# Performance work log

Hardware: AMD Instinct MI355X
Metric: run time of the kernel (lower is better)

## Reference

```python
import jax, jax.numpy as jnp
import numpy as np

B, S, D_IN, H = 64, 1024, 1024, 1024


def setup_inputs() -> dict:
    key = jax.random.key(0)
    ks = jax.random.split(key, 5)
    scale_x = 1.0 / np.sqrt(D_IN)
    scale_h = 1.0 / np.sqrt(H)
    # gate order along leading axis: f, i, o, g
    W = jax.random.uniform(ks[0], (4, D_IN, H), jnp.float32, -scale_x, scale_x)
    bW = jax.random.uniform(ks[1], (4, H), jnp.float32, -scale_x, scale_x)
    U = jax.random.uniform(ks[2], (4, H, H), jnp.float32, -scale_h, scale_h)
    bU = jax.random.uniform(ks[3], (4, H), jnp.float32, -scale_h, scale_h)
    input_emb = jax.random.normal(ks[4], (B, S, D_IN), jnp.float32)
    return {"input_emb": input_emb, "W": W, "bW": bW, "U": U, "bU": bU}


def reference(input_emb, W, bW, U, bU):
    b, s, _ = input_emb.shape
    h_dim = W.shape[-1]
    # Precompute input projections for all 4 gates across all timesteps: (S, B, 4, H)
    xproj = jnp.einsum('bsd,kdh->sbkh', input_emb, W) + bW

    def step(carry, xt):
        h_prev, c_prev = carry
        # recurrent projection for all gates: (B, 4, H)
        gates = xt + jnp.einsum('bh,kho->bko', h_prev, U) + bU
        f_t = jax.nn.sigmoid(gates[:, 0])
        i_t = jax.nn.sigmoid(gates[:, 1])
        o_t = jax.nn.sigmoid(gates[:, 2])
        g_t = jax.nn.sigmoid(gates[:, 3])  # NOTE: original uses sigmoid here, not tanh
        c_t = f_t * c_prev + i_t * g_t
        h_t = o_t * jnp.tanh(c_t)
        return (h_t, c_t), h_t

    h0 = jnp.zeros((b, h_dim), input_emb.dtype)
    c0 = jnp.zeros((b, h_dim), input_emb.dtype)
    (h_last, c_last), ys = jax.lax.scan(step, (h0, c0), xproj)
    outputs = jnp.transpose(ys, (1, 0, 2))  # (B, S, H)
    return outputs, (h_last, c_last)
```

## Files before the change

### kernel.cpp

```cpp
#include <hip/hip_runtime.h>
#include <hip/hip_bf16.h>
#include <stdint.h>


typedef __attribute__((ext_vector_type(8))) short short8;
typedef __attribute__((ext_vector_type(4))) float floatx4;
typedef __attribute__((ext_vector_type(2))) float floatx2;

__device__ __forceinline__ unsigned short f2bf(float x){
  union { float f; unsigned int u; } v; v.f = x;
  unsigned int r = v.u + 0x7fffu + ((v.u >> 16) & 1u);
  return (unsigned short)(r >> 16);
}
__device__ __forceinline__ float bf2f(unsigned short b){
  union { unsigned int u; float f; } v; v.u = ((unsigned int)b) << 16; return v.f;
}
__device__ __forceinline__ float fsigmoid(float x){ return 1.0f / (1.0f + __expf(-x)); }
__device__ __forceinline__ float ftanh(float x){ return 1.0f - 2.0f / (1.0f + __expf(2.0f * x)); }

__global__ void k_transpose_bf16(const float* __restrict__ src, unsigned short* __restrict__ dst){
  __shared__ float tile[64][65];
  const int g  = blockIdx.z;
  const int d0 = blockIdx.x * 64;
  const int h0 = blockIdx.y * 64;
  const int t  = threadIdx.x;
  const float* s    = src + ((size_t)g << 20);
  unsigned short* o = dst + ((size_t)g << 20);
  #pragma unroll
  for (int i = 0; i < 16; i++){
    int e = i * 256 + t;
    int r = e >> 6, c = e & 63;
    tile[r][c] = s[(size_t)(d0 + r) * 1024 + (h0 + c)];
  }
  __syncthreads();
  #pragma unroll
  for (int i = 0; i < 16; i++){
    int e = i * 256 + t;
    int a = e >> 6, bb = e & 63;
    o[(size_t)(h0 + a) * 1024 + (d0 + bb)] = f2bf(tile[bb][a]);
  }
}

__global__ void k_convert_x(const float* __restrict__ inp, unsigned short* __restrict__ abuf, int s0){
  int idx = blockIdx.x * 256 + threadIdx.x;
  int e = idx * 4;
  int r = e >> 10, d = e & 1023;
  int b = r & 63, sl = r >> 6;
  floatx4 v = *(const floatx4*)(inp + ((size_t)(b * 1024 + (s0 + sl)) * 1024 + d));
  unsigned long long pk = (unsigned long long)f2bf(v[0])
                        | ((unsigned long long)f2bf(v[1]) << 16)
                        | ((unsigned long long)f2bf(v[2]) << 32)
                        | ((unsigned long long)f2bf(v[3]) << 48);
  *(unsigned long long*)(abuf + (size_t)r * 1024 + d) = pk;
}

__global__ void __launch_bounds__(256) k_gemm_xproj(
    const unsigned short* __restrict__ A,
    const unsigned short* __restrict__ Bt,
    const float* __restrict__ bW,
    const float* __restrict__ bU,
    unsigned short* __restrict__ Cc)
{
  __shared__ unsigned short As[2][128][64];
  __shared__ unsigned short Bs[2][128][64];
  const int t = threadIdx.x;
  const int w = t >> 6;
  const int lane = t & 63;
  const int m0 = blockIdx.x * 128;
  const int n0 = blockIdx.y * 128;
  floatx4 acc[4][4];
  #pragma unroll
  for (int i = 0; i < 4; i++)
    #pragma unroll
    for (int j = 0; j < 4; j++)
      acc[i][j] = (floatx4){0.f, 0.f, 0.f, 0.f};

  auto stage = [&](int bufi, int kt){
    #pragma unroll
    for (int i = 0; i < 4; i++){
      int chunk = i * 256 + t;
      int r = chunk >> 3, j = chunk & 7;
      int js = j ^ (r & 7);
      __builtin_amdgcn_global_load_lds(
        (const __attribute__((address_space(1))) unsigned int*)(A + (size_t)(m0 + r) * 1024 + kt * 64 + js * 8),
        (__attribute__((address_space(3))) unsigned int*)(&As[bufi][0][0] + (i * 256 + w * 64) * 8), 16, 0, 0);
    }
    #pragma unroll
    for (int i = 0; i < 4; i++){
      int chunk = i * 256 + t;
      int r = chunk >> 3, j = chunk & 7;
      int js = j ^ (r & 7);
      __builtin_amdgcn_global_load_lds(
        (const __attribute__((address_space(1))) unsigned int*)(Bt + (size_t)(n0 + r) * 1024 + kt * 64 + js * 8),
        (__attribute__((address_space(3))) unsigned int*)(&Bs[bufi][0][0] + (i * 256 + w * 64) * 8), 16, 0, 0);
    }
  };

  auto compute = [&](int bufi){
    const int mi0 = (w >> 1) * 64;
    const int ni0 = (w & 1) * 64;
    #pragma unroll
    for (int kc = 0; kc < 2; kc++){
      short8 af[4], bfr[4];
      #pragma unroll
      for (int mi = 0; mi < 4; mi++){
        int row = mi0 + mi * 16 + (lane & 15);
        int j = kc * 4 + (lane >> 4);
        af[mi] = *(const short8*)&As[bufi][row][(j ^ (row & 7)) * 8];
      }
      #pragma unroll
      for (int ni = 0; ni < 4; ni++){
        int row = ni0 + ni * 16 + (lane & 15);
        int j = kc * 4 + (lane >> 4);
        bfr[ni] = *(const short8*)&Bs[bufi][row][(j ^ (row & 7)) * 8];
      }
      #pragma unroll
      for (int mi = 0; mi < 4; mi++)
        #pragma unroll
        for (int ni = 0; ni < 4; ni++)
          acc[mi][ni] = __builtin_amdgcn_mfma_f32_16x16x32_bf16(af[mi], bfr[ni], acc[mi][ni], 0, 0, 0);
    }
  };

  stage(0, 0);
  int buf = 0;
  for (int kt = 0; kt < 16; kt++){
    __syncthreads();
    if (kt < 15) stage(buf ^ 1, kt + 1);
    compute(buf);
    buf ^= 1;
  }

  {
    const int mi0 = (w >> 1) * 64;
    const int ni0 = (w & 1) * 64;
    #pragma unroll
    for (int ni = 0; ni < 4; ni++){
      int col = n0 + ni0 + ni * 16 + (lane & 15);
      float bias = bW[col] + bU[col];
      #pragma unroll
      for (int mi = 0; mi < 4; mi++){
        int mrow = m0 + mi0 + mi * 16 + (lane >> 4) * 4;
        #pragma unroll
        for (int r = 0; r < 4; r++)
          Cc[(size_t)(mrow + r) * 4096 + col] = f2bf(acc[mi][ni][r] + bias);
      }
    }
  }
}

__global__ void __launch_bounds__(256, 1) k_lstm_rec(
    const unsigned short* __restrict__ xp,
    const unsigned short* __restrict__ Ut,
    unsigned short* hbs,
    float* cstate,
    float* __restrict__ out,
    float* __restrict__ hlast,
    float* __restrict__ clast,
    int* flags,
    int s_base, int SC)
{
  const int t = threadIdx.x;
  const int w = t >> 6;
  const int lane = t & 63;
  const int wgid = blockIdx.x;
  const int g  = wgid & 3;
  const int j  = wgid >> 2;
  const int B0 = g * 16;
  const int gc0 = j * 32;

  __shared__ float glds[4][16][33];

  short8 bfrag0[32], bfrag1[32];
  {
    const unsigned short* bp0 = Ut + (size_t)(w * 1024 + gc0 + (lane & 15)) * 1024 + (lane >> 4) * 8;
    const unsigned short* bp1 = bp0 + (size_t)16 * 1024;
    #pragma unroll
    for (int kc = 0; kc < 32; kc++){
      bfrag0[kc] = *(const short8*)(bp0 + kc * 32);
      bfrag1[kc] = *(const short8*)(bp1 + kc * 32);
    }
  }

  const int b   = t >> 4;
  const int cc2 = (t & 15) * 2;
  floatx2 cst;
  if (s_base == 0) cst = (floatx2){0.f, 0.f};
  else             cst = *(const floatx2*)&cstate[(size_t)(B0 + b) * 1024 + gc0 + cc2];

  int bail = 20000000;
  const int fb = g * 32;

  for (int sl = 0; sl < SC; sl++){
    const int s = s_base + sl;
    const int p = s & 1;

    unsigned int xu[4];
    {
      const unsigned short* xr = xp + ((size_t)(sl * 64 + B0 + b)) * 4096 + gc0 + cc2;
      #pragma unroll
      for (int gg = 0; gg < 4; gg++) xu[gg] = *(const unsigned int*)(xr + gg * 1024);
    }
    __builtin_amdgcn_sched_barrier(0);

    const char* gsrc = (const char*)hbs + ((size_t)p * 4 + g) * 32768;
    floatx4 acc0 = (floatx4){0.f,0.f,0.f,0.f};
    floatx4 acc1 = (floatx4){0.f,0.f,0.f,0.f};

    auto wait_chunk = [&](int c){
      if (s == 0) return;
      const int* fp2 = &flags[fb + c * 8 + (lane & 7)];
      while (true){
        int v = __hip_atomic_load(fp2, __ATOMIC_RELAXED, __HIP_MEMORY_SCOPE_AGENT);
        if (__all(v >= s)) break;
        __builtin_amdgcn_s_sleep(1);
        if (--bail < 0) break;
      }
    };

    unsigned long long loA[8], hiA[8], loB[8], hiB[8];
    auto issue8 = [&](unsigned long long (&lo)[8], unsigned long long (&hi)[8], int ch){
      #pragma unroll
      for (int i = 0; i < 8; i++){
        const unsigned long long* sp2 = (const unsigned long long*)(gsrc + (ch * 8 + i) * 1024 + lane * 16);
        lo[i] = __hip_atomic_load(sp2,     __ATOMIC_RELAXED, __HIP_MEMORY_SCOPE_AGENT);
        hi[i] = __hip_atomic_load(sp2 + 1, __ATOMIC_RELAXED, __HIP_MEMORY_SCOPE_AGENT);
      }
    };
    auto crunch8 = [&](unsigned long long (&lo)[8], unsigned long long (&hi)[8], int ch){
      #pragma unroll
      for (int i = 0; i < 8; i++){
        union { unsigned long long q[2]; short8 v; } u;
        u.q[0] = lo[i]; u.q[1] = hi[i];
        acc0 = __builtin_amdgcn_mfma_f32_16x16x32_bf16(u.v, bfrag0[ch * 8 + i], acc0, 0, 0, 0);
        acc1 = __builtin_amdgcn_mfma_f32_16x16x32_bf16(u.v, bfrag1[ch * 8 + i], acc1, 0, 0, 0);
      }
    };
    wait_chunk(0);
    issue8(loA, hiA, 0);
    wait_chunk(1);
    issue8(loB, hiB, 1);
    crunch8(loA, hiA, 0);
    wait_chunk(2);
    issue8(loA, hiA, 2);
    crunch8(loB, hiB, 1);
    wait_chunk(3);
    issue8(loB, hiB, 3);
    crunch8(loA, hiA, 2);
    crunch8(loB, hiB, 3);

    {
      const int r0 = (lane >> 4) * 4;
      const int cl = lane & 15;
      #pragma unroll
      for (int r = 0; r < 4; r++){
        glds[w][r0 + r][cl]      = acc0[r];
        glds[w][r0 + r][16 + cl] = acc1[r];
      }
    }
    __syncthreads();

    float hout[2];
    #pragma unroll
    for (int d = 0; d < 2; d++){
      float fv = fsigmoid(glds[0][b][cc2 + d] + bf2f((unsigned short)(xu[0] >> (16 * d))));
      float iv = fsigmoid(glds[1][b][cc2 + d] + bf2f((unsigned short)(xu[1] >> (16 * d))));
      float ov = fsigmoid(glds[2][b][cc2 + d] + bf2f((unsigned short)(xu[2] >> (16 * d))));
      float gv = fsigmoid(glds[3][b][cc2 + d] + bf2f((unsigned short)(xu[3] >> (16 * d))));
      float cv = fv * cst[d] + iv * gv;
      cst[d] = cv;
      hout[d] = ov * ftanh(cv);
    }

    {
      unsigned int hv = (unsigned int)f2bf(hout[0]) | ((unsigned int)f2bf(hout[1]) << 16);
      unsigned int* dst = (unsigned int*)((char*)hbs + ((size_t)(p ^ 1) * 4 + g) * 32768 + j * 1024
                + (((cc2 >> 3) * 16 + b) << 4) + ((cc2 & 7) << 1));
      __hip_atomic_store(dst, hv, __ATOMIC_RELAXED, __HIP_MEMORY_SCOPE_AGENT);
    }

    if (s == 1023){
      *(floatx2*)&hlast[(size_t)(B0 + b) * 1024 + gc0 + cc2] = (floatx2){hout[0], hout[1]};
      *(floatx2*)&clast[(size_t)(B0 + b) * 1024 + gc0 + cc2] = cst;
    }

    asm volatile("s_waitcnt vmcnt(0)" ::: "memory");
    __syncthreads();
    if (t == 0)
      __hip_atomic_store(&flags[fb + j], s + 1, __ATOMIC_RELAXED, __HIP_MEMORY_SCOPE_AGENT);

    *(floatx2*)&out[((size_t)(B0 + b) * 1024 + s) * 1024 + gc0 + cc2] = (floatx2){hout[0], hout[1]};
  }

  *(floatx2*)&cstate[(size_t)(B0 + b) * 1024 + gc0 + cc2] = cst;
}

extern "C" void kernel_launch(void* const* d_in, const int* in_sizes, int n_in,
                              void* d_out, int out_size, void* d_ws, size_t ws_size,
                              hipStream_t stream)
{
  (void)in_sizes; (void)n_in; (void)out_size;
  const float* input_emb = (const float*)d_in[0];
  const float* W   = (const float*)d_in[1];
  const float* bWp = (const float*)d_in[2];
  const float* U   = (const float*)d_in[3];
  const float* bUp = (const float*)d_in[4];
  float* out   = (float*)d_out;
  float* hlast = out + (size_t)64 * 1024 * 1024;
  float* clast = hlast + 64 * 1024;

  char* base = (char*)d_ws;
  unsigned short* Wt  = (unsigned short*)base;  base += 8388608;
  unsigned short* Ut  = (unsigned short*)base;  base += 8388608;
  unsigned short* hbs = (unsigned short*)base;  base += 262144;
  float* cstate       = (float*)base;           base += 262144;
  int* flags          = (int*)base;             base += 8192;
  size_t fixed = (size_t)(base - (char*)d_ws);
  size_t avail = ws_size > fixed ? ws_size - fixed : 0;
  int SC = 1024;
  while (SC > 8 && (size_t)SC * 655360ull > avail) SC >>= 1;
  unsigned short* Abuf = (unsigned short*)base; base += (size_t)SC * 131072;
  unsigned short* xpb  = (unsigned short*)base;

  hipMemsetAsync(flags, 0, 8192, stream);
  hipMemsetAsync(hbs, 0, 262144, stream);

  k_transpose_bf16<<<dim3(16, 16, 4), 256, 0, stream>>>(W, Wt);
  k_transpose_bf16<<<dim3(16, 16, 4), 256, 0, stream>>>(U, Ut);

  int nch = 1024 / SC;
  for (int cc = 0; cc < nch; cc++){
    int s0 = cc * SC;
    k_convert_x<<<SC * 64, 256, 0, stream>>>(input_emb, Abuf, s0);
    k_gemm_xproj<<<dim3(SC / 2, 32), 256, 0, stream>>>(Abuf, Wt, bWp, bUp, xpb);
    k_lstm_rec<<<128, 256, 0, stream>>>(xpb, Ut, hbs, cstate, out, hlast, clast, flags, s0, SC);
  }
}
```

Baseline: 6.319 ms.

## Split recurrent LSTM across 256 workgroups with 16 hidden columns each

The persistent recurrent kernel now gives each workgroup 16 hidden columns instead of 32 and launches 256 workgroups instead of 128. This halves the register-resident U fragments and the MFMA work per workgroup per timestep, spreading the serial recurrence over more compute units. In exchange, each step waits on twice as many producer flags (16 per chunk instead of 8), and paired h values are packed with a lane shuffle before the store. It relies on all 256 workgroups being co-resident for the spin-wait synchronisation.

```diff
diff --git a/kernel.cpp b/kernel.cpp
--- a/kernel.cpp
+++ b/kernel.cpp
@@ -5,7 +5,6 @@
 
 typedef __attribute__((ext_vector_type(8))) short short8;
 typedef __attribute__((ext_vector_type(4))) float floatx4;
-typedef __attribute__((ext_vector_type(2))) float floatx2;
 
 __device__ __forceinline__ unsigned short f2bf(float x){
   union { float f; unsigned int u; } v; v.f = x;
@@ -167,55 +166,55 @@
   const int g  = wgid & 3;
   const int j  = wgid >> 2;
   const int B0 = g * 16;
-  const int gc0 = j * 32;
-
-  __shared__ float glds[4][16][33];
-
-  short8 bfrag0[32], bfrag1[32];
+  const int gc0 = j * 16;
+
+  __shared__ float glds[4][16][17];
+
+  short8 bfrag[32];
   {
-    const unsigned short* bp0 = Ut + (size_t)(w * 1024 + gc0 + (lane & 15)) * 1024 + (lane >> 4) * 8;
-    const unsigned short* bp1 = bp0 + (size_t)16 * 1024;
-    #pragma unroll
-    for (int kc = 0; kc < 32; kc++){
-      bfrag0[kc] = *(const short8*)(bp0 + kc * 32);
-      bfrag1[kc] = *(const short8*)(bp1 + kc * 32);
-    }
-  }
-
-  const int b   = t >> 4;
-  const int cc2 = (t & 15) * 2;
-  floatx2 cst;
-  if (s_base == 0) cst = (floatx2){0.f, 0.f};
-  else             cst = *(const floatx2*)&cstate[(size_t)(B0 + b) * 1024 + gc0 + cc2];
+    const unsigned short* bp = Ut + (size_t)(w * 1024 + gc0 + (lane & 15)) * 1024 + (lane >> 4) * 8;
+    #pragma unroll
+    for (int kc = 0; kc < 32; kc++)
+      bfrag[kc] = *(const short8*)(bp + kc * 32);
+  }
+
+  const int b  = t >> 4;
+  const int cc = t & 15;
+  float cst;
+  if (s_base == 0) cst = 0.f;
+  else             cst = cstate[(size_t)(B0 + b) * 1024 + gc0 + cc];
 
   int bail = 20000000;
-  const int fb = g * 32;
+  const int fb = g * 64;
 
   for (int sl = 0; sl < SC; sl++){
     const int s = s_base + sl;
     const int p = s & 1;
 
-    unsigned int xu[4];
+    unsigned short xv[4];
     {
-      const unsigned short* xr = xp + ((size_t)(sl * 64 + B0 + b)) * 4096 + gc0 + cc2;
-      #pragma unroll
-      for (int gg = 0; gg < 4; gg++) xu[gg] = *(const unsigned int*)(xr + gg * 1024);
+      const unsigned short* xr = xp + ((size_t)(sl * 64 + B0 + b)) * 4096 + gc0 + cc;
+      #pragma unroll
+      for (int gg = 0; gg < 4; gg++) xv[gg] = xr[gg * 1024];
     }
     __builtin_amdgcn_sched_barrier(0);
 
     const char* gsrc = (const char*)hbs + ((size_t)p * 4 + g) * 32768;
-    floatx4 acc0 = (floatx4){0.f,0.f,0.f,0.f};
-    floatx4 acc1 = (floatx4){0.f,0.f,0.f,0.f};
+    floatx4 acc = (floatx4){0.f,0.f,0.f,0.f};
 
     auto wait_chunk = [&](int c){
       if (s == 0) return;
-      const int* fp2 = &flags[fb + c * 8 + (lane & 7)];
       while (true){
-        int v = __hip_atomic_load(fp2, __ATOMIC_RELAXED, __HIP_MEMORY_SCOPE_AGENT);
-        if (__all(v >= s)) break;
+        bool ok = true;
+        if (lane < 16){
+          int v = __hip_atomic_load(&flags[fb + c * 16 + lane], __ATOMIC_RELAXED, __HIP_MEMORY_SCOPE_AGENT);
+          ok = (v >= s);
+        }
+        if (__all(ok)) break;
         __builtin_amdgcn_s_sleep(1);
         if (--bail < 0) break;
       }
+      asm volatile("" ::: "memory");
     };
 
     unsigned long long loA[8], hiA[8], loB[8], hiB[8];
@@ -232,10 +231,10 @@
       for (int i = 0; i < 8; i++){
         union { unsigned long long q[2]; short8 v; } u;
         u.q[0] = lo[i]; u.q[1] = hi[i];
-        acc0 = __builtin_amdgcn_mfma_f32_16x16x32_bf16(u.v, bfrag0[ch * 8 + i], acc0, 0, 0, 0);
-        acc1 = __builtin_amdgcn_mfma_f32_16x16x32_bf16(u.v, bfrag1[ch * 8 + i], acc1, 0, 0, 0);
+        acc = __builtin_amdgcn_mfma_f32_16x16x32_bf16(u.v, bfrag[ch * 8 + i], acc, 0, 0, 0);
       }
     };
+
     wait_chunk(0);
     issue8(loA, hiA, 0);
     wait_chunk(1);
@@ -253,35 +252,32 @@
       const int r0 = (lane >> 4) * 4;
       const int cl = lane & 15;
       #pragma unroll
-      for (int r = 0; r < 4; r++){
-        glds[w][r0 + r][cl]      = acc0[r];
-        glds[w][r0 + r][16 + cl] = acc1[r];
-      }
+      for (int r = 0; r < 4; r++)
+        glds[w][r0 + r][cl] = acc[r];
     }
     __syncthreads();
 
-    float hout[2];
-    #pragma unroll
-    for (int d = 0; d < 2; d++){
-      float fv = fsigmoid(glds[0][b][cc2 + d] + bf2f((unsigned short)(xu[0] >> (16 * d))));
-      float iv = fsigmoid(glds[1][b][cc2 + d] + bf2f((unsigned short)(xu[1] >> (16 * d))));
-      float ov = fsigmoid(glds[2][b][cc2 + d] + bf2f((unsigned short)(xu[2] >> (16 * d))));
-      float gv = fsigmoid(glds[3][b][cc2 + d] + bf2f((unsigned short)(xu[3] >> (16 * d))));
-      float cv = fv * cst[d] + iv * gv;
-      cst[d] = cv;
-      hout[d] = ov * ftanh(cv);
-    }
+    float fv = fsigmoid(glds[0][b][cc] + bf2f(xv[0]));
+    float iv = fsigmoid(glds[1][b][cc] + bf2f(xv[1]));
+    float ov = fsigmoid(glds[2][b][cc] + bf2f(xv[2]));
+    float gv = fsigmoid(glds[3][b][cc] + bf2f(xv[3]));
+    cst = fv * cst + iv * gv;
+    float hout = ov * ftanh(cst);
 
     {
-      unsigned int hv = (unsigned int)f2bf(hout[0]) | ((unsigned int)f2bf(hout[1]) << 16);
-      unsigned int* dst = (unsigned int*)((char*)hbs + ((size_t)(p ^ 1) * 4 + g) * 32768 + j * 1024
-                + (((cc2 >> 3) * 16 + b) << 4) + ((cc2 & 7) << 1));
-      __hip_atomic_store(dst, hv, __ATOMIC_RELAXED, __HIP_MEMORY_SCOPE_AGENT);
+      unsigned int my = (unsigned int)f2bf(hout);
+      unsigned int nb = __shfl_down(my, 1);
+      if (!(lane & 1)){
+        const int kl = ((j & 1) << 4) + cc;
+        unsigned int* dst = (unsigned int*)((char*)hbs + ((size_t)(p ^ 1) * 4 + g) * 32768
+                  + (size_t)(j >> 1) * 1024 + (((kl >> 3) * 16 + b) << 4) + ((kl & 7) << 1));
+        __hip_atomic_store(dst, my | (nb << 16), __ATOMIC_RELAXED, __HIP_MEMORY_SCOPE_AGENT);
+      }
     }
 
     if (s == 1023){
-      *(floatx2*)&hlast[(size_t)(B0 + b) * 1024 + gc0 + cc2] = (floatx2){hout[0], hout[1]};
-      *(floatx2*)&clast[(size_t)(B0 + b) * 1024 + gc0 + cc2] = cst;
+      hlast[(size_t)(B0 + b) * 1024 + gc0 + cc] = hout;
+      clast[(size_t)(B0 + b) * 1024 + gc0 + cc] = cst;
     }
 
     asm volatile("s_waitcnt vmcnt(0)" ::: "memory");
@@ -289,10 +285,10 @@
     if (t == 0)
       __hip_atomic_store(&flags[fb + j], s + 1, __ATOMIC_RELAXED, __HIP_MEMORY_SCOPE_AGENT);
 
-    *(floatx2*)&out[((size_t)(B0 + b) * 1024 + s) * 1024 + gc0 + cc2] = (floatx2){hout[0], hout[1]};
-  }
-
-  *(floatx2*)&cstate[(size_t)(B0 + b) * 1024 + gc0 + cc2] = cst;
+    out[((size_t)(B0 + b) * 1024 + s) * 1024 + gc0 + cc] = hout;
+  }
+
+  cstate[(size_t)(B0 + b) * 1024 + gc0 + cc] = cst;
 }
 
 extern "C" void kernel_launch(void* const* d_in, const int* in_sizes, int n_in,
@@ -333,6 +329,6 @@
     int s0 = cc * SC;
     k_convert_x<<<SC * 64, 256, 0, stream>>>(input_emb, Abuf, s0);
     k_gemm_xproj<<<dim3(SC / 2, 32), 256, 0, stream>>>(Abuf, Wt, bWp, bUp, xpb);
-    k_lstm_rec<<<128, 256, 0, stream>>>(xpb, Ut, hbs, cstate, out, hlast, clast, flags, s0, SC);
-  }
-}
+    k_lstm_rec<<<256, 256, 0, stream>>>(xpb, Ut, hbs, cstate, out, hlast, clast, flags, s0, SC);
+  }
+}
```

Result: slower. 6.999 ms (+10.8%).
